# Optimization experiments

Measured on AMD Instinct MI355X. Metric: run time of the kernel, lower is better.

The kernel has to match this reference:

```python
import jax, jax.numpy as jnp
import numpy as np

B, T, D, H = 4, 2048, 1024, 16
DK = D // H

def setup_inputs() -> dict:
    key = jax.random.key(0)
    k1, k2, k3 = jax.random.split(key, 3)
    s = 1.0 / np.sqrt(D)
    return {
        "x": jax.random.normal(k1, (B, T, D), dtype=jnp.float32),
        "W_qkv": jax.random.normal(k2, (D, 3 * D), dtype=jnp.float32) * s,
        "b_qkv": jnp.zeros((3 * D,), dtype=jnp.float32),
        "W_out": jax.random.normal(k3, (D, D), dtype=jnp.float32) * s,
        "b_out": jnp.zeros((D,), dtype=jnp.float32),
    }

def reference(x, W_qkv, b_qkv, W_out, b_out):
    Bx, Tx, C = x.shape
    qkv = x @ W_qkv + b_qkv                       # [B,T,3D]
    q, k, v = jnp.split(qkv, 3, axis=-1)
    # [B,T,D] -> [B,H,T,dk]
    def heads(t):
        return t.reshape(Bx, Tx, H, DK).transpose(0, 2, 1, 3)
    q, k, v = heads(q), heads(k), heads(v)
    scores = jnp.einsum('bhqd,bhkd->bhqk', q, k) / jnp.sqrt(jnp.float32(DK))
    causal = jnp.tril(jnp.ones((Tx, Tx), dtype=bool))  # [T,T]
    scores = jnp.where(causal[None, None], scores, -jnp.inf)
    attn = jax.nn.softmax(scores, axis=-1)        # dropout p=0 (eval)
    out = jnp.einsum('bhqk,bhkd->bhqd', attn, v)  # [B,H,T,dk]
    out = out.transpose(0, 2, 1, 3).reshape(Bx, Tx, C)
    return out @ W_out + b_out
```

## Files before the change

kernel.cpp:

```cpp
#include <hip/hip_runtime.h>
#include <hip/hip_bf16.h>
#include <stdint.h>

#define T_SEQ 2048
#define DMODEL 1024
#define NH 16
#define DKH 64
#define M_TOK 8192
#define N_QKV 3072
#define K_DIM 1024

typedef __attribute__((ext_vector_type(8))) short short8;
typedef __attribute__((ext_vector_type(4))) short short4v;
typedef __attribute__((ext_vector_type(4))) float float4v;

__device__ inline short bf16_bits(float f) {
  __hip_bfloat16 h = __float2bfloat16(f);
  short s;
  __builtin_memcpy(&s, &h, 2);
  return s;
}

__device__ inline void async_load16(const void* g, void* l) {
  __builtin_amdgcn_global_load_lds(
      (const __attribute__((address_space(1))) unsigned int*)g,
      (__attribute__((address_space(3))) unsigned int*)l,
      16, 0, 0);
}


__global__ __launch_bounds__(256) void cvt_kernel(const float* __restrict__ in,
                                                  short* __restrict__ out, int n) {
  int idx = (blockIdx.x * 256 + threadIdx.x) * 4;
  if (idx < n) {
    float4v v = *(const float4v*)(in + idx);
    short4v o;
    o[0] = bf16_bits(v[0]); o[1] = bf16_bits(v[1]);
    o[2] = bf16_bits(v[2]); o[3] = bf16_bits(v[3]);
    *(short4v*)(out + idx) = o;
  }
}

__global__ __launch_bounds__(256) void transpose_cvt(const float* __restrict__ in,
                                                     short* __restrict__ out,
                                                     int K, int N) {
  __shared__ float tile[32][33];
  int n0 = blockIdx.x * 32, k0 = blockIdx.y * 32;
  int tx = threadIdx.x, ty = threadIdx.y;
  #pragma unroll
  for (int r = ty; r < 32; r += 8)
    tile[r][tx] = in[(size_t)(k0 + r) * N + n0 + tx];
  __syncthreads();
  #pragma unroll
  for (int r = ty; r < 32; r += 8)
    out[(size_t)(n0 + r) * K + k0 + tx] = bf16_bits(tile[tx][r]);
}


template <int MODE>
__global__ __launch_bounds__(256) void gemm_bt(
    const short* __restrict__ A, const short* __restrict__ Bt,
    const float* __restrict__ bias,
    short* __restrict__ Qb, short* __restrict__ Kb, short* __restrict__ Vt,
    float* __restrict__ Cout, int M, int N, int K) {
  __shared__ __align__(16) short As[128 * 32];
  __shared__ __align__(16) short Bs[128 * 32];
  const int tid = threadIdx.x;
  const int lane = tid & 63;
  const int wave = tid >> 6;
  const int m0 = blockIdx.y * 128;
  const int n0 = blockIdx.x * 128;
  const int wm = (wave >> 1) * 64;
  const int wn = (wave & 1) * 64;
  const int quad = lane >> 4;
  const int l16 = lane & 15;

  float4v acc[4][4] = {};

  const int r0 = tid >> 2,        o0 = (tid & 3) * 8;
  const int r1 = (tid + 256) >> 2, o1 = ((tid + 256) & 3) * 8;
  short* ldsA0 = As + (size_t)(wave * 64) * 8;
  short* ldsA1 = As + (size_t)(256 + wave * 64) * 8;
  short* ldsB0 = Bs + (size_t)(wave * 64) * 8;
  short* ldsB1 = Bs + (size_t)(256 + wave * 64) * 8;

  for (int kt = 0; kt < K; kt += 32) {
    async_load16(A  + (size_t)(m0 + r0) * K + kt + o0, ldsA0);
    async_load16(A  + (size_t)(m0 + r1) * K + kt + o1, ldsA1);
    async_load16(Bt + (size_t)(n0 + r0) * K + kt + o0, ldsB0);
    async_load16(Bt + (size_t)(n0 + r1) * K + kt + o1, ldsB1);
    __builtin_amdgcn_s_waitcnt(0);
    __syncthreads();

    short8 af[4], bfr[4];
    #pragma unroll
    for (int t = 0; t < 4; ++t)
      af[t] = *(const short8*)(As + (size_t)(wm + t * 16 + l16) * 32 + quad * 8);
    #pragma unroll
    for (int t = 0; t < 4; ++t)
      bfr[t] = *(const short8*)(Bs + (size_t)(wn + t * 16 + l16) * 32 + quad * 8);
    #pragma unroll
    for (int i = 0; i < 4; ++i)
      #pragma unroll
      for (int j = 0; j < 4; ++j)
        acc[i][j] = __builtin_amdgcn_mfma_f32_16x16x32_bf16(af[i], bfr[j], acc[i][j], 0, 0, 0);
    __syncthreads();
  }

  if (MODE == 0) {
    #pragma unroll
    for (int tj = 0; tj < 4; ++tj) {
      int col = n0 + wn + tj * 16 + l16;
      float bz = bias[col];
      int which = col >> 10;
      int d = col & 1023;
      int h = d >> 6, dk = d & 63;
      #pragma unroll
      for (int ti = 0; ti < 4; ++ti) {
        int rbase = m0 + wm + ti * 16 + quad * 4;
        int b = rbase >> 11;
        int t = rbase & 2047;
        if (which == 2) {
          short4v pv;
          #pragma unroll
          for (int i = 0; i < 4; ++i) pv[i] = bf16_bits(acc[ti][tj][i] + bz);
          int c = (t >> 3) & 7;
          int tp = (t & ~63) | ((((c + dk) & 7) << 3)) | (t & 7);
          *(short4v*)(Vt + ((size_t)(b * NH + h) * DKH + dk) * T_SEQ + tp) = pv;
        } else if (which == 0) {
          #pragma unroll
          for (int i = 0; i < 4; ++i)
            Qb[((size_t)(b * NH + h) * T_SEQ + t + i) * DKH + dk] =
                bf16_bits(acc[ti][tj][i] + bz);
        } else {
          #pragma unroll
          for (int i = 0; i < 4; ++i) {
            int tt = t + i;
            int dkp = ((((dk >> 3) + tt) & 7) << 3) | (dk & 7);
            Kb[((size_t)(b * NH + h) * T_SEQ + tt) * DKH + dkp] =
                bf16_bits(acc[ti][tj][i] + bz);
          }
        }
      }
    }
  } else {
    #pragma unroll
    for (int tj = 0; tj < 4; ++tj) {
      int col = n0 + wn + tj * 16 + l16;
      float bz = bias[col];
      #pragma unroll
      for (int ti = 0; ti < 4; ++ti)
        #pragma unroll
        for (int i = 0; i < 4; ++i) {
          int row = m0 + wm + ti * 16 + quad * 4 + i;
          Cout[(size_t)row * N + col] = acc[ti][tj][i] + bz;
        }
    }
  }
}


__global__ __launch_bounds__(256) void attn_kernel(const short* __restrict__ Qb,
                                                   const short* __restrict__ Kb,
                                                   const short* __restrict__ Vt,
                                                   short* __restrict__ Ao) {
  __shared__ __align__(16) short KsB[2][64 * 64];
  __shared__ __align__(16) short VsB[2][64 * 64];
  const int bh = blockIdx.x;
  const int qb = 15 - blockIdx.y;
  const int tid = threadIdx.x;
  const int lane = tid & 63, wave = tid >> 6;
  const int quad = lane >> 4, l16 = lane & 15;
  const int qw0 = qb * 128 + wave * 32;
  const int nkb = 2 * qb + 2;

  const short* Qg = Qb + ((size_t)bh * T_SEQ + qw0) * DKH;
  const short* Kg0 = Kb + (size_t)bh * T_SEQ * DKH;
  const short* Vg0 = Vt + (size_t)bh * DKH * T_SEQ;

  short8 aq[2][2];
  #pragma unroll
  for (int qi = 0; qi < 2; ++qi)
    #pragma unroll
    for (int h = 0; h < 2; ++h)
      aq[qi][h] = *(const short8*)(Qg + (size_t)(qi * 16 + l16) * DKH + h * 32 + quad * 8);

  float4v oc[2][4] = {};
  float l_i[2] = {0.f, 0.f};

  const float SC = 0.125f * 1.44269504f;
  const int vrow = tid >> 3, vcol = (tid & 7) * 8;
  const int sK0 = ((quad + l16) & 7) << 3;
  const int sK1 = ((quad + 4 + l16) & 7) << 3;

  async_load16(Kg0 + tid * 8,        &KsB[0][0] + wave * 512);
  async_load16(Kg0 + 2048 + tid * 8, &KsB[0][0] + 2048 + wave * 512);
  async_load16(Vg0 + (size_t)vrow * T_SEQ + vcol,        &VsB[0][0] + wave * 512);
  async_load16(Vg0 + (size_t)(32 + vrow) * T_SEQ + vcol, &VsB[0][0] + 2048 + wave * 512);

  for (int kb = 0; kb < nkb; ++kb) {
    const int k0 = kb * 64;
    __builtin_amdgcn_s_waitcnt(0);
    __syncthreads();

    if (kb + 1 < nkb) {
      const int kn = k0 + 64;
      const int nb = (kb + 1) & 1;
      const short* Kg = Kg0 + (size_t)kn * DKH;
      async_load16(Kg + tid * 8,        &KsB[nb][0] + wave * 512);
      async_load16(Kg + 2048 + tid * 8, &KsB[nb][0] + 2048 + wave * 512);
      async_load16(Vg0 + (size_t)vrow * T_SEQ + kn + vcol,        &VsB[nb][0] + wave * 512);
      async_load16(Vg0 + (size_t)(32 + vrow) * T_SEQ + kn + vcol, &VsB[nb][0] + 2048 + wave * 512);
    }

    if (k0 <= qw0 + 31) {
      const short* Ks = &KsB[kb & 1][0];
      const short* Vs = &VsB[kb & 1][0];
      const bool need_mask = (k0 + 63 > qw0);
      float rs[2] = {0.f, 0.f};

      #pragma unroll
      for (int c = 0; c < 4; ++c) {
        const int r = c * 16 + l16;
        short8 b0 = *(const short8*)(Ks + r * 64 + sK0);
        short8 b1 = *(const short8*)(Ks + r * 64 + sK1);
        short4v vf[4];
        #pragma unroll
        for (int d = 0; d < 4; ++d) {
          const int pos = ((c * 2 + (quad >> 1) + l16) & 7) * 8 + (quad & 3 & 1) * 4;
          vf[d] = *(const short4v*)(Vs + (d * 16 + l16) * 64 + pos);
        }
        #pragma unroll
        for (int qi = 0; qi < 2; ++qi) {
          float4v z = {0.f, 0.f, 0.f, 0.f};
          z = __builtin_amdgcn_mfma_f32_16x16x32_bf16(b0, aq[qi][0], z, 0, 0, 0);
          z = __builtin_amdgcn_mfma_f32_16x16x32_bf16(b1, aq[qi][1], z, 0, 0, 0);
          short4v pb;
          #pragma unroll
          for (int i = 0; i < 4; ++i) {
            float p = exp2f(z[i] * SC);
            if (need_mask && (k0 + c * 16 + quad * 4 + i > qw0 + qi * 16 + l16))
              p = 0.f;
            rs[qi] += p;
            pb[i] = bf16_bits(p);
          }
          #pragma unroll
          for (int d = 0; d < 4; ++d)
            oc[qi][d] = __builtin_amdgcn_mfma_f32_16x16x16bf16_1k(vf[d], pb, oc[qi][d], 0, 0, 0);
        }
      }
      #pragma unroll
      for (int qi = 0; qi < 2; ++qi) {
        float v = rs[qi];
        v += __shfl_xor(v, 16, 64);
        v += __shfl_xor(v, 32, 64);
        l_i[qi] += v;
      }
    }
  }

  const int b = bh >> 4, h = bh & 15;
  #pragma unroll
  for (int qi = 0; qi < 2; ++qi) {
    float rl = 1.0f / l_i[qi];
    #pragma unroll
    for (int d = 0; d < 4; ++d) {
      short4v o;
      #pragma unroll
      for (int i = 0; i < 4; ++i) o[i] = bf16_bits(oc[qi][d][i] * rl);
      int t = qw0 + qi * 16 + l16;
      *(short4v*)(Ao + (size_t)(b * T_SEQ + t) * DMODEL + h * DKH + d * 16 + quad * 4) = o;
    }
  }
}


extern "C" void kernel_launch(void* const* d_in, const int* in_sizes, int n_in,
                              void* d_out, int out_size, void* d_ws, size_t ws_size,
                              hipStream_t stream) {
  const float* x    = (const float*)d_in[0];
  const float* Wqkv = (const float*)d_in[1];
  const float* bqkv = (const float*)d_in[2];
  const float* Wout = (const float*)d_in[3];
  const float* bout = (const float*)d_in[4];
  float* out = (float*)d_out;

  char* ws = (char*)d_ws;
  short* Xb    = (short*)(ws);
  short* Wqkvt = (short*)(ws + (16ull << 20));
  short* Woutt = (short*)(ws + (22ull << 20));
  short* Qb    = (short*)(ws + (24ull << 20));
  short* Kb    = (short*)(ws + (40ull << 20));
  short* Vt    = (short*)(ws + (56ull << 20));
  short* Ao    = (short*)(ws + (72ull << 20));

  cvt_kernel<<<(M_TOK * K_DIM / 4 + 255) / 256, 256, 0, stream>>>(x, Xb, M_TOK * K_DIM);
  dim3 tb(32, 8);
  transpose_cvt<<<dim3(N_QKV / 32, K_DIM / 32), tb, 0, stream>>>(Wqkv, Wqkvt, K_DIM, N_QKV);
  transpose_cvt<<<dim3(DMODEL / 32, K_DIM / 32), tb, 0, stream>>>(Wout, Woutt, K_DIM, DMODEL);

  gemm_bt<0><<<dim3(N_QKV / 128, M_TOK / 128), 256, 0, stream>>>(
      Xb, Wqkvt, bqkv, Qb, Kb, Vt, nullptr, M_TOK, N_QKV, K_DIM);

  attn_kernel<<<dim3(64, T_SEQ / 128), 256, 0, stream>>>(Qb, Kb, Vt, Ao);

  gemm_bt<1><<<dim3(DMODEL / 128, M_TOK / 128), 256, 0, stream>>>(
      Ao, Woutt, bout, nullptr, nullptr, nullptr, out, M_TOK, DMODEL, K_DIM);
}
```

Measured before the change: 287.1 us.

## Store K/V in MFMA fragment order and compute row sums via MFMA

The QKV GEMM epilogue now writes K and V into per-64-token tiles laid out in the exact fragment order the attention MFMAs consume. The attention kernel can then load each operand with one contiguous LDS read per lane, with no swizzle arithmetic. Row sums of the softmax numerators are accumulated by an extra MFMA against a ones vector, replacing the per-lane adds and cross-lane shuffles. Masked and unmasked tiles are split into template specialisations, and probabilities are packed to bf16 two at a time. The trade-offs are an extra MFMA per step and scattered 2-byte stores in the K epilogue.

```diff
diff --git a/kernel.cpp b/kernel.cpp
--- a/kernel.cpp
+++ b/kernel.cpp
@@ -10,15 +10,28 @@
 #define N_QKV 3072
 #define K_DIM 1024
 
+#define ATTN_SC (0.125f * 1.44269504f)
+
 typedef __attribute__((ext_vector_type(8))) short short8;
 typedef __attribute__((ext_vector_type(4))) short short4v;
 typedef __attribute__((ext_vector_type(4))) float float4v;
+typedef __attribute__((ext_vector_type(2))) unsigned int uint2v;
 
 __device__ inline short bf16_bits(float f) {
   __hip_bfloat16 h = __float2bfloat16(f);
   short s;
   __builtin_memcpy(&s, &h, 2);
   return s;
+}
+
+__device__ inline short4v pack4_bf16(float a, float b, float c, float d) {
+  __hip_bfloat162 h0 = __float22bfloat162_rn(make_float2(a, b));
+  __hip_bfloat162 h1 = __float22bfloat162_rn(make_float2(c, d));
+  unsigned int u0, u1;
+  __builtin_memcpy(&u0, &h0, 4);
+  __builtin_memcpy(&u1, &h1, 4);
+  uint2v uu = {u0, u1};
+  return __builtin_bit_cast(short4v, uu);
 }
 
 __device__ inline void async_load16(const void* g, void* l) {
@@ -61,7 +74,7 @@
 __global__ __launch_bounds__(256) void gemm_bt(
     const short* __restrict__ A, const short* __restrict__ Bt,
     const float* __restrict__ bias,
-    short* __restrict__ Qb, short* __restrict__ Kb, short* __restrict__ Vt,
+    short* __restrict__ Qb, short* __restrict__ Kf, short* __restrict__ Vf,
     float* __restrict__ Cout, int M, int N, int K) {
   __shared__ __align__(16) short As[128 * 32];
   __shared__ __align__(16) short Bs[128 * 32];
@@ -120,26 +133,27 @@
         int rbase = m0 + wm + ti * 16 + quad * 4;
         int b = rbase >> 11;
         int t = rbase & 2047;
+        size_t bhoff = (size_t)(b * NH + h) * (T_SEQ * DKH);
         if (which == 2) {
           short4v pv;
           #pragma unroll
           for (int i = 0; i < 4; ++i) pv[i] = bf16_bits(acc[ti][tj][i] + bz);
-          int c = (t >> 3) & 7;
-          int tp = (t & ~63) | ((((c + dk) & 7) << 3)) | (t & 7);
-          *(short4v*)(Vt + ((size_t)(b * NH + h) * DKH + dk) * T_SEQ + tp) = pv;
+          size_t off = bhoff + (size_t)(t >> 6) * 4096 +
+                       ((((t >> 4) & 3) * 4 + (dk >> 4)) * 4 + ((t >> 2) & 3)) * 64 +
+                       (dk & 15) * 4;
+          *(short4v*)(Vf + off) = pv;
         } else if (which == 0) {
           #pragma unroll
           for (int i = 0; i < 4; ++i)
-            Qb[((size_t)(b * NH + h) * T_SEQ + t + i) * DKH + dk] =
-                bf16_bits(acc[ti][tj][i] + bz);
+            Qb[bhoff + (size_t)(t + i) * DKH + dk] = bf16_bits(acc[ti][tj][i] + bz);
         } else {
+          int h2 = dk >> 5, qd = (dk >> 3) & 3, w = dk & 7;
+          size_t kbase = bhoff + (size_t)(t >> 6) * 4096 +
+                         ((((t >> 4) & 3) * 2 + h2) * 4 + qd) * 128 + w;
+          int lb = t & 15;
           #pragma unroll
-          for (int i = 0; i < 4; ++i) {
-            int tt = t + i;
-            int dkp = ((((dk >> 3) + tt) & 7) << 3) | (dk & 7);
-            Kb[((size_t)(b * NH + h) * T_SEQ + tt) * DKH + dkp] =
-                bf16_bits(acc[ti][tj][i] + bz);
-          }
+          for (int i = 0; i < 4; ++i)
+            Kf[kbase + (lb + i) * 8] = bf16_bits(acc[ti][tj][i] + bz);
         }
       }
     }
@@ -160,12 +174,47 @@
 }
 
 
+template <int MASK>
+__device__ __forceinline__ void attn_tile(
+    const short* __restrict__ Ks, const short* __restrict__ Vs,
+    const short8 aq[2][2], short4v ones,
+    float4v oc[2][4], float4v lc[2],
+    int dkq, int quad, int l16) {
+  const int mb = dkq + quad * 4 - l16;
+  #pragma unroll
+  for (int c = 0; c < 4; ++c) {
+    short8 b0 = *(const short8*)(Ks + (c * 2 + 0) * 512 + quad * 128 + l16 * 8);
+    short8 b1 = *(const short8*)(Ks + (c * 2 + 1) * 512 + quad * 128 + l16 * 8);
+    short4v vf[4];
+    #pragma unroll
+    for (int d = 0; d < 4; ++d)
+      vf[d] = *(const short4v*)(Vs + (c * 4 + d) * 256 + quad * 64 + l16 * 4);
+    #pragma unroll
+    for (int qi = 0; qi < 2; ++qi) {
+      float4v z = {0.f, 0.f, 0.f, 0.f};
+      z = __builtin_amdgcn_mfma_f32_16x16x32_bf16(b0, aq[qi][0], z, 0, 0, 0);
+      z = __builtin_amdgcn_mfma_f32_16x16x32_bf16(b1, aq[qi][1], z, 0, 0, 0);
+      float p[4];
+      #pragma unroll
+      for (int i = 0; i < 4; ++i) {
+        p[i] = exp2f(z[i] * ATTN_SC);
+        if (MASK && (mb + c * 16 + i - qi * 16 > 0)) p[i] = 0.f;
+      }
+      short4v pb = pack4_bf16(p[0], p[1], p[2], p[3]);
+      lc[qi] = __builtin_amdgcn_mfma_f32_16x16x16bf16_1k(ones, pb, lc[qi], 0, 0, 0);
+      #pragma unroll
+      for (int d = 0; d < 4; ++d)
+        oc[qi][d] = __builtin_amdgcn_mfma_f32_16x16x16bf16_1k(vf[d], pb, oc[qi][d], 0, 0, 0);
+    }
+  }
+}
+
 __global__ __launch_bounds__(256) void attn_kernel(const short* __restrict__ Qb,
-                                                   const short* __restrict__ Kb,
-                                                   const short* __restrict__ Vt,
+                                                   const short* __restrict__ Kf,
+                                                   const short* __restrict__ Vf,
                                                    short* __restrict__ Ao) {
-  __shared__ __align__(16) short KsB[2][64 * 64];
-  __shared__ __align__(16) short VsB[2][64 * 64];
+  __shared__ __align__(16) short KsB[2][4096];
+  __shared__ __align__(16) short VsB[2][4096];
   const int bh = blockIdx.x;
   const int qb = 15 - blockIdx.y;
   const int tid = threadIdx.x;
@@ -175,8 +224,8 @@
   const int nkb = 2 * qb + 2;
 
   const short* Qg = Qb + ((size_t)bh * T_SEQ + qw0) * DKH;
-  const short* Kg0 = Kb + (size_t)bh * T_SEQ * DKH;
-  const short* Vg0 = Vt + (size_t)bh * DKH * T_SEQ;
+  const short* Kg0 = Kf + (size_t)bh * (T_SEQ * DKH);
+  const short* Vg0 = Vf + (size_t)bh * (T_SEQ * DKH);
 
   short8 aq[2][2];
   #pragma unroll
@@ -186,83 +235,40 @@
       aq[qi][h] = *(const short8*)(Qg + (size_t)(qi * 16 + l16) * DKH + h * 32 + quad * 8);
 
   float4v oc[2][4] = {};
-  float l_i[2] = {0.f, 0.f};
-
-  const float SC = 0.125f * 1.44269504f;
-  const int vrow = tid >> 3, vcol = (tid & 7) * 8;
-  const int sK0 = ((quad + l16) & 7) << 3;
-  const int sK1 = ((quad + 4 + l16) & 7) << 3;
+  float4v lc[2] = {};
+  short4v ones = {0x3F80, 0x3F80, 0x3F80, 0x3F80};
 
   async_load16(Kg0 + tid * 8,        &KsB[0][0] + wave * 512);
   async_load16(Kg0 + 2048 + tid * 8, &KsB[0][0] + 2048 + wave * 512);
-  async_load16(Vg0 + (size_t)vrow * T_SEQ + vcol,        &VsB[0][0] + wave * 512);
-  async_load16(Vg0 + (size_t)(32 + vrow) * T_SEQ + vcol, &VsB[0][0] + 2048 + wave * 512);
+  async_load16(Vg0 + tid * 8,        &VsB[0][0] + wave * 512);
+  async_load16(Vg0 + 2048 + tid * 8, &VsB[0][0] + 2048 + wave * 512);
 
   for (int kb = 0; kb < nkb; ++kb) {
-    const int k0 = kb * 64;
     __builtin_amdgcn_s_waitcnt(0);
     __syncthreads();
 
     if (kb + 1 < nkb) {
-      const int kn = k0 + 64;
       const int nb = (kb + 1) & 1;
-      const short* Kg = Kg0 + (size_t)kn * DKH;
+      const short* Kg = Kg0 + (size_t)(kb + 1) * 4096;
+      const short* Vg = Vg0 + (size_t)(kb + 1) * 4096;
       async_load16(Kg + tid * 8,        &KsB[nb][0] + wave * 512);
       async_load16(Kg + 2048 + tid * 8, &KsB[nb][0] + 2048 + wave * 512);
-      async_load16(Vg0 + (size_t)vrow * T_SEQ + kn + vcol,        &VsB[nb][0] + wave * 512);
-      async_load16(Vg0 + (size_t)(32 + vrow) * T_SEQ + kn + vcol, &VsB[nb][0] + 2048 + wave * 512);
-    }
-
-    if (k0 <= qw0 + 31) {
-      const short* Ks = &KsB[kb & 1][0];
-      const short* Vs = &VsB[kb & 1][0];
-      const bool need_mask = (k0 + 63 > qw0);
-      float rs[2] = {0.f, 0.f};
-
-      #pragma unroll
-      for (int c = 0; c < 4; ++c) {
-        const int r = c * 16 + l16;
-        short8 b0 = *(const short8*)(Ks + r * 64 + sK0);
-        short8 b1 = *(const short8*)(Ks + r * 64 + sK1);
-        short4v vf[4];
-        #pragma unroll
-        for (int d = 0; d < 4; ++d) {
-          const int pos = ((c * 2 + (quad >> 1) + l16) & 7) * 8 + (quad & 3 & 1) * 4;
-          vf[d] = *(const short4v*)(Vs + (d * 16 + l16) * 64 + pos);
-        }
-        #pragma unroll
-        for (int qi = 0; qi < 2; ++qi) {
-          float4v z = {0.f, 0.f, 0.f, 0.f};
-          z = __builtin_amdgcn_mfma_f32_16x16x32_bf16(b0, aq[qi][0], z, 0, 0, 0);
-          z = __builtin_amdgcn_mfma_f32_16x16x32_bf16(b1, aq[qi][1], z, 0, 0, 0);
-          short4v pb;
-          #pragma unroll
-          for (int i = 0; i < 4; ++i) {
-            float p = exp2f(z[i] * SC);
-            if (need_mask && (k0 + c * 16 + quad * 4 + i > qw0 + qi * 16 + l16))
-              p = 0.f;
-            rs[qi] += p;
-            pb[i] = bf16_bits(p);
-          }
-          #pragma unroll
-          for (int d = 0; d < 4; ++d)
-            oc[qi][d] = __builtin_amdgcn_mfma_f32_16x16x16bf16_1k(vf[d], pb, oc[qi][d], 0, 0, 0);
-        }
-      }
-      #pragma unroll
-      for (int qi = 0; qi < 2; ++qi) {
-        float v = rs[qi];
-        v += __shfl_xor(v, 16, 64);
-        v += __shfl_xor(v, 32, 64);
-        l_i[qi] += v;
-      }
+      async_load16(Vg + tid * 8,        &VsB[nb][0] + wave * 512);
+      async_load16(Vg + 2048 + tid * 8, &VsB[nb][0] + 2048 + wave * 512);
+    }
+
+    const int dkq = kb * 64 - qw0;
+    if (dkq + 63 <= 0) {
+      attn_tile<0>(&KsB[kb & 1][0], &VsB[kb & 1][0], aq, ones, oc, lc, dkq, quad, l16);
+    } else if (dkq <= 31) {
+      attn_tile<1>(&KsB[kb & 1][0], &VsB[kb & 1][0], aq, ones, oc, lc, dkq, quad, l16);
     }
   }
 
   const int b = bh >> 4, h = bh & 15;
   #pragma unroll
   for (int qi = 0; qi < 2; ++qi) {
-    float rl = 1.0f / l_i[qi];
+    float rl = 1.0f / lc[qi][0];
     #pragma unroll
     for (int d = 0; d < 4; ++d) {
       short4v o;
@@ -290,8 +296,8 @@
   short* Wqkvt = (short*)(ws + (16ull << 20));
   short* Woutt = (short*)(ws + (22ull << 20));
   short* Qb    = (short*)(ws + (24ull << 20));
-  short* Kb    = (short*)(ws + (40ull << 20));
-  short* Vt    = (short*)(ws + (56ull << 20));
+  short* Kf    = (short*)(ws + (40ull << 20));
+  short* Vf    = (short*)(ws + (56ull << 20));
   short* Ao    = (short*)(ws + (72ull << 20));
 
   cvt_kernel<<<(M_TOK * K_DIM / 4 + 255) / 256, 256, 0, stream>>>(x, Xb, M_TOK * K_DIM);
@@ -300,9 +306,9 @@
   transpose_cvt<<<dim3(DMODEL / 32, K_DIM / 32), tb, 0, stream>>>(Wout, Woutt, K_DIM, DMODEL);
 
   gemm_bt<0><<<dim3(N_QKV / 128, M_TOK / 128), 256, 0, stream>>>(
-      Xb, Wqkvt, bqkv, Qb, Kb, Vt, nullptr, M_TOK, N_QKV, K_DIM);
-
-  attn_kernel<<<dim3(64, T_SEQ / 128), 256, 0, stream>>>(Qb, Kb, Vt, Ao);
+      Xb, Wqkvt, bqkv, Qb, Kf, Vf, nullptr, M_TOK, N_QKV, K_DIM);
+
+  attn_kernel<<<dim3(64, T_SEQ / 128), 256, 0, stream>>>(Qb, Kf, Vf, Ao);
 
   gemm_bt<1><<<dim3(DMODEL / 128, M_TOK / 128), 256, 0, stream>>>(
       Ao, Woutt, bout, nullptr, nullptr, nullptr, out, M_TOK, DMODEL, K_DIM);
```

Result: no change. 287.1 us (-0.0%).
